# Kernel tuning notes

Hardware: AMD Instinct MI355X
Metric: run time of the kernel (lower is better)

## Reference

```python
import jax, jax.numpy as jnp
import numpy as np

B, T, D = 2, 512, 1024
H = 16
DH = D // H          # 64 head dim
E = 8                # experts
K = 2                # top-k routing
F = 4 * D            # expert hidden dim


def _layernorm(x, s, b, eps=1e-5):
    mu = jnp.mean(x, axis=-1, keepdims=True)
    var = jnp.var(x, axis=-1, keepdims=True)
    return (x - mu) * jax.lax.rsqrt(var + eps) * s + b


def setup_inputs() -> dict:
    key = jax.random.key(0)
    ks = jax.random.split(key, 16)
    sd = 0.02
    return {
        "x": jax.random.normal(ks[0], (B, T, D), jnp.float32),
        "text_state": jax.random.normal(ks[1], (B, D), jnp.float32),
        "ln1_s": jnp.ones((D,), jnp.float32),
        "ln1_b": jnp.zeros((D,), jnp.float32),
        "w_qkv": jax.random.normal(ks[2], (D, 3 * D), jnp.float32) * sd,
        "b_qkv": jnp.zeros((3 * D,), jnp.float32),
        "w_o": jax.random.normal(ks[3], (D, D), jnp.float32) * sd,
        "b_o": jnp.zeros((D,), jnp.float32),
        "rel_bias": jax.random.normal(ks[4], (H, 2 * T - 1), jnp.float32) * sd,
        "ln2_s": jnp.ones((D,), jnp.float32),
        "ln2_b": jnp.zeros((D,), jnp.float32),
        "w_txt": jax.random.normal(ks[5], (D, D), jnp.float32) * sd,
        "b_txt": jnp.zeros((D,), jnp.float32),
        "w_r": jax.random.normal(ks[6], (D, E), jnp.float32) * sd,
        "b_r": jnp.zeros((E,), jnp.float32),
        "w1": jax.random.normal(ks[7], (E, D, F), jnp.float32) * sd,
        "b1": jnp.zeros((E, F), jnp.float32),
        "w2": jax.random.normal(ks[8], (E, F, D), jnp.float32) * sd,
        "b2": jnp.zeros((E, D), jnp.float32),
    }


def reference(x, text_state, ln1_s, ln1_b, w_qkv, b_qkv, w_o, b_o, rel_bias,
              ln2_s, ln2_b, w_txt, b_txt, w_r, b_r, w1, b1, w2, b2):
    # ---- temporal-bias multi-head self-attention (pre-LN, residual) ----
    h = _layernorm(x, ln1_s, ln1_b)
    qkv = (h @ w_qkv + b_qkv).reshape(B, T, 3, H, DH)
    q, k, v = qkv[:, :, 0], qkv[:, :, 1], qkv[:, :, 2]       # [B,T,H,DH]
    scores = jnp.einsum("bthd,bshd->bhts", q, k) / np.sqrt(DH).astype(np.float32)
    idx = jnp.arange(T)
    rel = idx[None, :] - idx[:, None] + (T - 1)              # [T,T] in [0, 2T-2]
    scores = scores + rel_bias[:, rel][None]                 # broadcast [1,H,T,T]
    attn = jax.nn.softmax(scores, axis=-1)
    ctx = jnp.einsum("bhts,bshd->bthd", attn, v).reshape(B, T, D)
    x = x + ctx @ w_o + b_o

    # ---- top-k MoE feed-forward with text-conditioned router ----
    h2 = _layernorm(x, ln2_s, ln2_b)
    router_in = h2 + (text_state @ w_txt + b_txt)[:, None, :]
    probs = jax.nn.softmax(router_in @ w_r + b_r, axis=-1)   # [B,T,E]
    topv, topi = jax.lax.top_k(probs, K)                     # [B,T,K]
    gates = topv / jnp.sum(topv, axis=-1, keepdims=True)
    gates_full = jnp.einsum("btk,btke->bte", gates, jax.nn.one_hot(topi, E, dtype=x.dtype))
    # dense grouped-expert compute, sparsely combined (same math as dispatch)
    hid = jax.nn.gelu(jnp.einsum("btd,edf->btef", h2, w1) + b1)      # [B,T,E,F]
    eout = jnp.einsum("btef,efd->bted", hid, w2) + b2                # [B,T,E,D]
    y = jnp.einsum("bte,bted->btd", gates_full, eout)
    x = x + y

    diag = jnp.mean(probs, axis=(0, 1))                      # expert load [E]
    return x, diag
```

## Files before the change

kernel.cpp:

```cpp
#include <hip/hip_runtime.h>
#include <hip/hip_bf16.h>
#include <math.h>

#define BB 2
#define TT 512
#define DD 1024
#define HH 16
#define DHH 64
#define EE 8
#define FF 4096
#define NTOK 1024
#define CAP 3072
#define SPL 2

typedef __attribute__((ext_vector_type(4))) float f32x4;
typedef __attribute__((ext_vector_type(8))) short short8;

__device__ __forceinline__ short f2b(float f) {
    __hip_bfloat16 h = __float2bfloat16(f);
    return *reinterpret_cast<short*>(&h);
}
__device__ __forceinline__ float b2f(short s) {
    __hip_bfloat16 h = *reinterpret_cast<__hip_bfloat16*>(&s);
    return __bfloat162float(h);
}

__device__ __forceinline__ void gload16(const short* g, short* l) {
    __builtin_amdgcn_global_load_lds((const __attribute__((address_space(1))) unsigned int*)g,
                                     (__attribute__((address_space(3))) unsigned int*)l,
                                     16, 0, 0);
}

template <int BF>
__global__ __launch_bounds__(256) void ln_kernel(const float* __restrict__ x,
                                                 const float* __restrict__ s,
                                                 const float* __restrict__ b,
                                                 void* __restrict__ outp) {
    int row = blockIdx.x;
    int tid = threadIdx.x;
    const float* xr = x + (size_t)row * DD;
    float sm = 0.f, sq = 0.f;
    for (int i = tid; i < DD; i += 256) {
        float v = xr[i];
        sm += v; sq += v * v;
    }
    #pragma unroll
    for (int o = 32; o; o >>= 1) {
        sm += __shfl_down(sm, o);
        sq += __shfl_down(sq, o);
    }
    __shared__ float r1[4], r2[4];
    if ((tid & 63) == 0) { r1[tid >> 6] = sm; r2[tid >> 6] = sq; }
    __syncthreads();
    float tot  = r1[0] + r1[1] + r1[2] + r1[3];
    float totq = r2[0] + r2[1] + r2[2] + r2[3];
    float mu  = tot * (1.f / DD);
    float var = totq * (1.f / DD) - mu * mu;
    float inv = rsqrtf(var + 1e-5f);
    for (int i = tid; i < DD; i += 256) {
        float v = (xr[i] - mu) * inv * s[i] + b[i];
        if (BF) ((short*)outp)[(size_t)row * DD + i] = f2b(v);
        else    ((float*)outp)[(size_t)row * DD + i] = v;
    }
}

__global__ __launch_bounds__(256) void transpose_cast(const float* __restrict__ src,
                                                      short* __restrict__ dst,
                                                      int K, int N) {
    __shared__ float t[64][65];
    src += (size_t)blockIdx.z * K * N;
    dst += (size_t)blockIdx.z * K * N;
    int k0 = blockIdx.y * 64, n0 = blockIdx.x * 64;
    int rr = threadIdx.x >> 4;
    int cc = (threadIdx.x & 15) * 4;
    #pragma unroll
    for (int p = 0; p < 4; p++) {
        float4 v = *(const float4*)&src[(size_t)(k0 + rr + p * 16) * N + n0 + cc];
        t[rr + p * 16][cc]     = v.x;
        t[rr + p * 16][cc + 1] = v.y;
        t[rr + p * 16][cc + 2] = v.z;
        t[rr + p * 16][cc + 3] = v.w;
    }
    __syncthreads();
    #pragma unroll
    for (int p = 0; p < 4; p++) {
        int n = rr + p * 16;
        short4 o;
        o.x = f2b(t[cc][n]); o.y = f2b(t[cc + 1][n]);
        o.z = f2b(t[cc + 2][n]); o.w = f2b(t[cc + 3][n]);
        *(short4*)&dst[(size_t)(n0 + n) * K + k0 + cc] = o;
    }
}

__global__ __launch_bounds__(256) void v_transpose(const short* __restrict__ Vb,
                                                   short* __restrict__ VTb) {
    __shared__ short t[32][33];
    int bh = blockIdx.z;
    const short* src = Vb + (size_t)bh * TT * DHH;
    short* dst = VTb + (size_t)bh * DHH * TT;
    int t0 = blockIdx.x * 32, d0 = blockIdx.y * 32;
    int tx = threadIdx.x & 31, ty = threadIdx.x >> 5;
    #pragma unroll
    for (int p = 0; p < 4; p++)
        t[ty + p * 8][tx] = src[(size_t)(t0 + ty + p * 8) * DHH + d0 + tx];
    __syncthreads();
    #pragma unroll
    for (int p = 0; p < 4; p++)
        dst[(size_t)(d0 + ty + p * 8) * TT + t0 + tx] = t[tx][ty + p * 8];
}

__device__ __forceinline__ void gemm_loop128(const short* __restrict__ A,
                                             const short* __restrict__ B,
                                             int K, int lda, int ldb,
                                             short* As, short* Bs,
                                             f32x4 acc[4][4], int m0, int n0, int tid) {
    int wave = tid >> 6, lane = tid & 63;
    int wr = wave >> 1, wc = wave & 1;
    int lrow = lane & 15, lk = lane >> 4;
    int srow = lane >> 3;
    int sslot = (lane & 7) ^ srow;
    const short* Agb = A + (size_t)(m0 + srow) * lda + sslot * 8;
    const short* Bgb = B + (size_t)(n0 + srow) * ldb + sslot * 8;
    for (int k0 = 0; k0 < K; k0 += 64) {
        #pragma unroll
        for (int p = 0; p < 4; p++) {
            int rg = (wave * 4 + p) * 8;
            gload16(Agb + (size_t)rg * lda + k0, As + rg * 64);
            gload16(Bgb + (size_t)rg * ldb + k0, Bs + rg * 64);
        }
        __syncthreads();
        #pragma unroll
        for (int kk = 0; kk < 2; kk++) {
            int q = kk * 4 + lk;
            short8 a[4], b[4];
            #pragma unroll
            for (int i = 0; i < 4; i++) {
                int r = wr * 64 + i * 16 + lrow;
                uint4 v = ((const uint4*)As)[r * 8 + (q ^ (r & 7))];
                a[i] = *(short8*)&v;
            }
            #pragma unroll
            for (int j = 0; j < 4; j++) {
                int r = wc * 64 + j * 16 + lrow;
                uint4 v = ((const uint4*)Bs)[r * 8 + (q ^ (r & 7))];
                b[j] = *(short8*)&v;
            }
            #pragma unroll
            for (int i = 0; i < 4; i++)
                #pragma unroll
                for (int j = 0; j < 4; j++)
                    acc[i][j] = __builtin_amdgcn_mfma_f32_16x16x32_bf16(a[i], b[j], acc[i][j], 0, 0, 0);
        }
        __syncthreads();
    }
}

__device__ __forceinline__ void gemm_loop64(const short* __restrict__ A,
                                            const short* __restrict__ B,
                                            int K, int lda, int ldb,
                                            short* As, short* Bs,
                                            f32x4 acc[2][2], int m0, int n0, int tid) {
    int wave = tid >> 6, lane = tid & 63;
    int wr = wave >> 1, wc = wave & 1;
    int lrow = lane & 15, lk = lane >> 4;
    int sr = tid >> 3, ss = tid & 7;
    int sswz = (ss ^ (sr & 7)) * 8;
    const short* Ag0 = A + (size_t)(m0 + sr) * lda + sswz;
    const short* Ag1 = A + (size_t)(m0 + sr + 32) * lda + sswz;
    const short* Bg0 = B + (size_t)(n0 + sr) * ldb + sswz;
    const short* Bg1 = B + (size_t)(n0 + sr + 32) * ldb + sswz;
    short* lA0 = As + wave * 512;
    short* lA1 = As + 2048 + wave * 512;
    short* lB0 = Bs + wave * 512;
    short* lB1 = Bs + 2048 + wave * 512;
    int nt = K >> 6;
    gload16(Ag0, lA0); gload16(Ag1, lA1);
    gload16(Bg0, lB0); gload16(Bg1, lB1);
    __syncthreads();
    for (int t = 0; t < nt; ++t) {
        int h = (t & 1) * 4096;
        if (t + 1 < nt) {
            int k0 = (t + 1) << 6;
            int hn = 4096 - h;
            gload16(Ag0 + k0, lA0 + hn); gload16(Ag1 + k0, lA1 + hn);
            gload16(Bg0 + k0, lB0 + hn); gload16(Bg1 + k0, lB1 + hn);
        }
        const uint4* Asc = (const uint4*)(As + h);
        const uint4* Bsc = (const uint4*)(Bs + h);
        #pragma unroll
        for (int kk = 0; kk < 2; kk++) {
            int slot = kk * 4 + lk;
// ... 39 lines not shown
    short* lA1 = As + 2048 + wave * 512;
    short* lB0 = Bs + wave * 512;
    short* lB1 = Bs + 2048 + wave * 512;
    short* lB2 = Bs + 4096 + wave * 512;
    short* lB3 = Bs + 6144 + wave * 512;
    int nt = K >> 6;
    gload16(Ag0, lA0); gload16(Ag1, lA1);
    gload16(Bg0, lB0); gload16(Bg1, lB1);
    gload16(Bg2, lB2); gload16(Bg3, lB3);
    __syncthreads();
    for (int t = 0; t < nt; ++t) {
        int hA = (t & 1) * 4096;
        int hB = (t & 1) * 8192;
        if (t + 1 < nt) {
            int k0 = (t + 1) << 6;
            int hnA = 4096 - hA, hnB = 8192 - hB;
            gload16(Ag0 + k0, lA0 + hnA); gload16(Ag1 + k0, lA1 + hnA);
            gload16(Bg0 + k0, lB0 + hnB); gload16(Bg1 + k0, lB1 + hnB);
            gload16(Bg2 + k0, lB2 + hnB); gload16(Bg3 + k0, lB3 + hnB);
        }
        const uint4* Asc = (const uint4*)(As + hA);
        const uint4* Bsc = (const uint4*)(Bs + hB);
        #pragma unroll
        for (int kk = 0; kk < 2; kk++) {
            int slot = kk * 4 + lk;
            short8 a[2], b[4];
            #pragma unroll
            for (int i = 0; i < 2; i++) {
                int row = wr * 32 + i * 16 + lrow;
                uint4 v = Asc[row * 8 + (slot ^ (row & 7))];
                a[i] = *(short8*)&v;
            }
            #pragma unroll
            for (int j = 0; j < 4; j++) {
                int row = wc * 64 + j * 16 + lrow;
                uint4 v = Bsc[row * 8 + (slot ^ (row & 7))];
                b[j] = *(short8*)&v;
            }
            #pragma unroll
            for (int i = 0; i < 2; i++)
                #pragma unroll
                for (int j = 0; j < 4; j++)
                    acc[i][j] = __builtin_amdgcn_mfma_f32_16x16x32_bf16(a[i], b[j], acc[i][j], 0, 0, 0);
        }
        __syncthreads();
    }
}

__global__ __launch_bounds__(256) void gemm64_res_mfma(const short* __restrict__ A,
                                                       const short* __restrict__ Bw,
                                                       const float* __restrict__ bias,
                                                       const float* __restrict__ res,
                                                       float* __restrict__ C,
                                                       int N, int K) {
    __shared__ short As[8192];
    __shared__ short Bs[8192];
    int tid = threadIdx.x;
    int m0 = blockIdx.y * 64, n0 = blockIdx.x * 64;
    f32x4 acc[2][2] = {};
    gemm_loop64(A, Bw, K, K, K, As, Bs, acc, m0, n0, tid);
    int wave = tid >> 6, lane = tid & 63;
    int wr = wave >> 1, wc = wave & 1;
    int lrow = lane & 15, lk = lane >> 4;
    #pragma unroll
    for (int i = 0; i < 2; i++) {
        #pragma unroll
        for (int j = 0; j < 2; j++) {
            int col = n0 + wc * 32 + j * 16 + lrow;
            float bv = bias[col];
            #pragma unroll
            for (int r = 0; r < 4; r++) {
                int row = m0 + wr * 32 + i * 16 + lk * 4 + r;
                C[(size_t)row * N + col] = acc[i][j][r] + bv + res[(size_t)row * N + col];
            }
        }
    }
}

__global__ __launch_bounds__(256) void qkv_mfma(const short* __restrict__ A,
                                                const short* __restrict__ Bw,
                                                const float* __restrict__ bias,
                                                short* __restrict__ Qb,
                                                short* __restrict__ Kb,
                                                short* __restrict__ Vb) {
    __shared__ short As[8192];
    __shared__ short Bs[16384];
    int tid = threadIdx.x;
    int m0 = blockIdx.y * 64, n0 = blockIdx.x * 128;
    f32x4 acc[2][4] = {};
    gemm_loop_w(A, Bw, DD, As, Bs, acc, m0, n0, tid);
    int wave = tid >> 6, lane = tid & 63;
    int wr = wave >> 1, wc = wave & 1;
    int lrow = lane & 15, lk = lane >> 4;
    #pragma unroll
    for (int i = 0; i < 2; i++) {
        #pragma unroll
        for (int j = 0; j < 4; j++) {
            int col = n0 + wc * 64 + j * 16 + lrow;
            int part = col >> 10;
            int rem = col & 1023;
            int h = rem >> 6, d = rem & 63;
            short* dst = (part == 0) ? Qb : ((part == 1) ? Kb : Vb);
            float bv = bias[col];
            #pragma unroll
            for (int r = 0; r < 4; r++) {
                int row = m0 + wr * 32 + i * 16 + lk * 4 + r;
                int b = row >> 9, t = row & (TT - 1);
                dst[(((size_t)(b * HH + h)) * TT + t) * DHH + d] = f2b(acc[i][j][r] + bv);
            }
        }
    }
}

__global__ __launch_bounds__(256) void scores_mfma(const short* __restrict__ Qb,
                                                   const short* __restrict__ Kb,
                                                   float* __restrict__ S) {
    __shared__ short As[8192];
    __shared__ short Bs[16384];
    int tid = threadIdx.x;
    int bh = blockIdx.z;
    const short* A = Qb + (size_t)bh * TT * DHH;
    const short* B = Kb + (size_t)bh * TT * DHH;
    float* Sp = S + (size_t)bh * TT * TT;
    int m0 = blockIdx.y * 64, n0 = blockIdx.x * 128;
    f32x4 acc[2][4] = {};
    gemm_loop_w(A, B, DHH, As, Bs, acc, m0, n0, tid);
    int wave = tid >> 6, lane = tid & 63;
    int wr = wave >> 1, wc = wave & 1;
    int lrow = lane & 15, lk = lane >> 4;
    #pragma unroll
    for (int i = 0; i < 2; i++)
        #pragma unroll
        for (int j = 0; j < 4; j++) {
            int col = n0 + wc * 64 + j * 16 + lrow;
            #pragma unroll
            for (int r = 0; r < 4; r++) {
                int row = m0 + wr * 32 + i * 16 + lk * 4 + r;
                Sp[(size_t)row * TT + col] = acc[i][j][r];
            }
        }
}

__global__ __launch_bounds__(256) void softmax_kernel(const float* __restrict__ S,
                                                      const float* __restrict__ rel_bias,
                                                      short* __restrict__ P) {
    int row = blockIdx.x * 4 + (threadIdx.x >> 6);
    int lane = threadIdx.x & 63;
    int t = row & (TT - 1), h = (row >> 9) & (HH - 1);
    const float* Sr = S + (size_t)row * TT;
    const float* br = rel_bias + h * (2 * TT - 1) + (TT - 1) - t;
    float v[8];
    float mx = -1e30f;
    #pragma unroll
    for (int i = 0; i < 8; i++) {
        int s = lane + i * 64;
        v[i] = Sr[s] * 0.125f + br[s];
        mx = fmaxf(mx, v[i]);
    }
    #pragma unroll
    for (int o = 32; o; o >>= 1) mx = fmaxf(mx, __shfl_xor(mx, o));
    float sum = 0.f;
    #pragma unroll
    for (int i = 0; i < 8; i++) { v[i] = expf(v[i] - mx); sum += v[i]; }
    #pragma unroll
    for (int o = 32; o; o >>= 1) sum += __shfl_xor(sum, o);
    float inv = 1.f / sum;
    #pragma unroll
    for (int i = 0; i < 8; i++)
        P[(size_t)row * TT + lane + i * 64] = f2b(v[i] * inv);
}

__global__ __launch_bounds__(256) void pv_mfma(const short* __restrict__ P,
                                               const short* __restrict__ VTb,
                                               short* __restrict__ ctxb) {
    __shared__ short As[8192];
    __shared__ short Bs[8192];
    int tid = threadIdx.x;
    int bh = blockIdx.z;
    int h = bh & (HH - 1), b = bh >> 4;
    const short* A = P + (size_t)bh * TT * TT;
    const short* B = VTb + (size_t)bh * DHH * TT;
    int m0 = blockIdx.y * 64;
    f32x4 acc[2][2] = {};
    gemm_loop64(A, B, TT, TT, TT, As, Bs, acc, m0, 0, tid);
    int wave = tid >> 6, lane = tid & 63;
    int wr = wave >> 1, wc = wave & 1;
    int lrow = lane & 15, lk = lane >> 4;
    #pragma unroll
    for (int i = 0; i < 2; i++)
        #pragma unroll
        for (int j = 0; j < 2; j++) {
            int d = wc * 32 + j * 16 + lrow;
            #pragma unroll
            for (int r = 0; r < 4; r++) {
                int row = m0 + wr * 32 + i * 16 + lk * 4 + r;
                ctxb[((size_t)(b * TT + row)) * DD + h * DHH + d] = f2b(acc[i][j][r]);
            }
        }
}

__global__ __launch_bounds__(256) void moe_gemm1_mfma(const short* __restrict__ Ag,
                                                      const short* __restrict__ W1t,
                                                      const float* __restrict__ b1,
                                                      const int* __restrict__ counts,
                                                      const int* __restrict__ offs,
                                                      short* __restrict__ hid) {
    int e = blockIdx.y >> 4, tile = blockIdx.y & 15;
    int cnt = counts[e];
    int pcnt = (cnt + 127) & ~127;
    int row0 = tile * 128;
    if (row0 >= pcnt) return;
    int base = offs[e];
    const short* A  = Ag + (size_t)base * DD;
    const short* Bw = W1t + (size_t)e * FF * DD;
    __shared__ short As[8192];
    __shared__ short Bs[8192];
    int tid = threadIdx.x;
    int n0 = blockIdx.x * 128;
    f32x4 acc[4][4] = {};
    gemm_loop128(A, Bw, DD, DD, DD, As, Bs, acc, row0, n0, tid);
    int wave = tid >> 6, lane = tid & 63;
    int wr = wave >> 1, wc = wave & 1;
    int lrow = lane & 15, lk = lane >> 4;
    #pragma unroll
    for (int i = 0; i < 4; i++) {
        #pragma unroll
        for (int j = 0; j < 4; j++) {
            int col = n0 + wc * 64 + j * 16 + lrow;
            float bv = b1[e * FF + col];
            #pragma unroll
            for (int r = 0; r < 4; r++) {
                int row = row0 + wr * 64 + i * 16 + lk * 4 + r;
                float v = acc[i][j][r] + bv;
                float u = 0.7978845608028654f * (v + 0.044715f * v * v * v);
                float g = 0.5f * v * (1.f + tanhf(u));
                hid[(size_t)(base + row) * FF + col] = f2b(g);
            }
        }
    }
}

__global__ __launch_bounds__(256) void moe_gemm2_mfma(const short* __restrict__ hid,
                                                      const short* __restrict__ W2t,
                                                      const float* __restrict__ b2,
                                                      const float* __restrict__ pair_gate,
                                                      const int* __restrict__ counts,
                                                      const int* __restrict__ offs,
                                                      short* __restrict__ pair_part) {
    int s = blockIdx.z;
    int e = blockIdx.y >> 4, tile = blockIdx.y & 15;
    int cnt = counts[e];
    int pcnt = (cnt + 127) & ~127;
    int row0 = tile * 128;
    if (row0 >= pcnt) return;
    int base = offs[e];
    const int KS = FF / SPL;
    const short* A  = hid + (size_t)base * FF + s * KS;
    const short* Bw = W2t + (size_t)e * DD * FF + s * KS;
    __shared__ short As[8192];
    __shared__ short Bs[8192];
    int tid = threadIdx.x;
    int n0 = blockIdx.x * 128;
    f32x4 acc[4][4] = {};
    gemm_loop128(A, Bw, KS, FF, FF, As, Bs, acc, row0, n0, tid);
    int wave = tid >> 6, lane = tid & 63;
    int wr = wave >> 1, wc = wave & 1;
    int lrow = lane & 15, lk = lane >> 4;
    #pragma unroll
    for (int i = 0; i < 4; i++) {
        #pragma unroll
        for (int j = 0; j < 4; j++) {
            int col = n0 + wc * 64 + j * 16 + lrow;
            float bv = (s == 0) ? b2[e * DD + col] : 0.f;
            #pragma unroll
            for (int r = 0; r < 4; r++) {
                int row = row0 + wr * 64 + i * 16 + lk * 4 + r;
                float g = pair_gate[base + row];
                pair_part[((size_t)s * CAP + base + row) * DD + col] = f2b(g * (acc[i][j][r] + bv));
            }
        }
    }
}

__global__ __launch_bounds__(256) void txt_kernel(const float* __restrict__ ts,
                                                  const float* __restrict__ w,
                                                  const float* __restrict__ bias,
                                                  float* __restrict__ out) {
    int b = blockIdx.y;
    int col = blockIdx.x * 32 + (threadIdx.x & 31);
    int dg = threadIdx.x >> 5;
    float acc = 0.f;
    for (int d = dg * 128; d < dg * 128 + 128; d++)
        acc += ts[b * DD + d] * w[(size_t)d * DD + col];
    __shared__ float red[8][32];
    red[dg][threadIdx.x & 31] = acc;
    __syncthreads();
    if (threadIdx.x < 32) {
        float s = 0.f;
        #pragma unroll
        for (int g = 0; g < 8; g++) s += red[g][threadIdx.x];
        out[b * DD + col] = s + bias[col];
    }
}

__global__ __launch_bounds__(256) void router_kernel(const float* __restrict__ h2,
                                                     const float* __restrict__ txt,
                                                     const float* __restrict__ w_r,
                                                     const float* __restrict__ b_r,
                                                     float* __restrict__ probs,
                                                     float* __restrict__ gates,
                                                     int* __restrict__ counts) {
    int row = blockIdx.x;
    int b = row >> 9;
    int tid = threadIdx.x;
    float acc[EE] = {};
    for (int d = tid; d < DD; d += 256) {
        float r = h2[(size_t)row * DD + d] + txt[b * DD + d];
        #pragma unroll
        for (int e = 0; e < EE; e++) acc[e] += r * w_r[d * EE + e];
    }
    #pragma unroll
    for (int e = 0; e < EE; e++)
        #pragma unroll
        for (int o = 32; o; o >>= 1) acc[e] += __shfl_down(acc[e], o);
    __shared__ float lds[4][EE];
    int lane = tid & 63, w = tid >> 6;
    if (lane == 0)
        for (int e = 0; e < EE; e++) lds[w][e] = acc[e];
    __syncthreads();
    if (tid == 0) {
        float lg[EE], p[EE];
        float mx = -1e30f;
        for (int e = 0; e < EE; e++) {
            lg[e] = lds[0][e] + lds[1][e] + lds[2][e] + lds[3][e] + b_r[e];
            mx = fmaxf(mx, lg[e]);
        }
        float sum = 0.f;
        for (int e = 0; e < EE; e++) { p[e] = expf(lg[e] - mx); sum += p[e]; }
        float invs = 1.f / sum;
        for (int e = 0; e < EE; e++) { p[e] *= invs; probs[row * EE + e] = p[e]; }
        int i1 = 0;
        for (int e = 1; e < EE; e++) if (p[e] > p[i1]) i1 = e;
        int i2 = (i1 == 0) ? 1 : 0;
        for (int e = 0; e < EE; e++) if (e != i1 && p[e] > p[i2]) i2 = e;
        float gs = p[i1] + p[i2];
        for (int e = 0; e < EE; e++) gates[row * EE + e] = 0.f;
        gates[row * EE + i1] = p[i1] / gs;
        gates[row * EE + i2] = p[i2] / gs;
        atomicAdd(&counts[i1], 1);
        atomicAdd(&counts[i2], 1);
    }
}

__global__ void offs_kernel(const int* __restrict__ counts, int* __restrict__ offs) {
    if (threadIdx.x == 0) {
        int acc = 0;
        for (int e = 0; e < EE; e++) { offs[e] = acc; acc += (counts[e] + 127) & ~127; }
    }
}

__global__ __launch_bounds__(256) void scatter_kernel(const float* __restrict__ gates,
                                                      const int* __restrict__ offs,
                                                      int* __restrict__ fill,
                                                      int* __restrict__ tok_pos,
                                                      float* __restrict__ pair_gate) {
    int t = blockIdx.x * 256 + threadIdx.x;
    if (t >= NTOK) return;
    int slot = 0;
    for (int e = 0; e < EE; e++) {
        float g = gates[t * EE + e];
        if (g > 0.f) {
            int pos = offs[e] + atomicAdd(&fill[e], 1);
            tok_pos[t * 2 + slot] = pos;
            pair_gate[pos] = g;
            slot++;
        }
    }
}

__global__ __launch_bounds__(256) void gather_tokens(const float* __restrict__ h2,
                                                     const int* __restrict__ tok_pos,
                                                     short* __restrict__ Ag) {
    int i = blockIdx.x;
    int pos = tok_pos[i];
    int t = i >> 1;
    int d = threadIdx.x * 4;
    #pragma unroll
    for (int k = 0; k < 4; k++)
        Ag[(size_t)pos * DD + d + k] = f2b(h2[(size_t)t * DD + d + k]);
}

__global__ __launch_bounds__(256) void diag_kernel(const float* __restrict__ probs,
                                                   float* __restrict__ out) {
    int e = blockIdx.x;
    int tid = threadIdx.x;
    float s = 0.f;
    for (int t = tid; t < NTOK; t += 256) s += probs[t * EE + e];
    #pragma unroll
    for (int o = 32; o; o >>= 1) s += __shfl_down(s, o);
    __shared__ float red[4];
    if ((tid & 63) == 0) red[tid >> 6] = s;
    __syncthreads();
    if (tid == 0) out[e] = (red[0] + red[1] + red[2] + red[3]) * (1.f / NTOK);
}

__global__ __launch_bounds__(256) void finaladd_kernel(float* __restrict__ out,
                                                       const short* __restrict__ pair_part,
                                                       const int* __restrict__ tok_pos) {
    int t = blockIdx.x;
    int d = threadIdx.x * 4;
    float4 a = *(const float4*)&out[(size_t)t * DD + d];
    #pragma unroll
    for (int sl = 0; sl < 2; sl++) {
        int pos = tok_pos[2 * t + sl];
        #pragma unroll
        for (int s = 0; s < SPL; s++) {
            short4 v = *(const short4*)&pair_part[((size_t)s * CAP + pos) * DD + d];
            a.x += b2f(v.x); a.y += b2f(v.y); a.z += b2f(v.z); a.w += b2f(v.w);
        }
    }
    *(float4*)&out[(size_t)t * DD + d] = a;
}

extern "C" void kernel_launch(void* const* d_in, const int* in_sizes, int n_in,
                              void* d_out, int out_size, void* d_ws, size_t ws_size,
                              hipStream_t stream) {
    const float* x          = (const float*)d_in[0];
    const float* text_state = (const float*)d_in[1];
    const float* ln1_s      = (const float*)d_in[2];
    const float* ln1_b      = (const float*)d_in[3];
    const float* w_qkv      = (const float*)d_in[4];
    const float* b_qkv      = (const float*)d_in[5];
    const float* w_o        = (const float*)d_in[6];
    const float* b_o        = (const float*)d_in[7];
    const float* rel_bias   = (const float*)d_in[8];
    const float* ln2_s      = (const float*)d_in[9];
    const float* ln2_b      = (const float*)d_in[10];
    const float* w_txt      = (const float*)d_in[11];
    const float* b_txt      = (const float*)d_in[12];
    const float* w_r        = (const float*)d_in[13];
    const float* b_r        = (const float*)d_in[14];
    const float* w1         = (const float*)d_in[15];
    const float* b1         = (const float*)d_in[16];
    const float* w2         = (const float*)d_in[17];
    const float* b2         = (const float*)d_in[18];

    float* out = (float*)d_out;

    char* p = (char*)d_ws;
    auto alloc = [&](size_t bytes) { char* r = p; p += (bytes + 255) & ~(size_t)255; return r; };
    short* h1b      = (short*)alloc((size_t)NTOK * DD * 2);
    short* Qb       = (short*)alloc((size_t)NTOK * DD * 2);
    short* Kb       = (short*)alloc((size_t)NTOK * DD * 2);
    short* Vb       = (short*)alloc((size_t)NTOK * DD * 2);
    short* VTb      = (short*)alloc((size_t)NTOK * DD * 2);
    char*  region1  = alloc((size_t)BB * HH * TT * TT * 4);
    char*  region2  = alloc((size_t)BB * HH * TT * TT * 2);
    short* ctxb     = (short*)alloc((size_t)NTOK * DD * 2);
    float* h2       = (float*)alloc((size_t)NTOK * DD * 4);
    float* txt      = (float*)alloc((size_t)BB * DD * 4);
    float* probs    = (float*)alloc((size_t)NTOK * EE * 4);
    float* gates    = (float*)alloc((size_t)NTOK * EE * 4);
    float* pair_gate= (float*)alloc((size_t)CAP * 4);
    int*   counts   = (int*)alloc(8 * 4);
    int*   fill     = (int*)alloc(8 * 4);
    int*   offs     = (int*)alloc(8 * 4);
    int*   tok_pos  = (int*)alloc((size_t)NTOK * 2 * 4);
    short* wqkvT    = (short*)alloc((size_t)3 * DD * DD * 2);
    short* woT      = (short*)alloc((size_t)DD * DD * 2);
    short* w1T      = (short*)alloc((size_t)EE * FF * DD * 2);
    short* w2T      = (short*)alloc((size_t)EE * DD * FF * 2);

    float* S         = (float*)region1;
    short* P         = (short*)region2;
    short* Ag        = (short*)region1;
    short* hid       = (short*)(region1 + (((size_t)CAP * DD * 2 + 255) & ~(size_t)255));
    short* pair_part = (short*)region2;

    transpose_cast<<<dim3(3 * DD / 64, DD / 64, 1), 256, 0, stream>>>(w_qkv, wqkvT, DD, 3 * DD);
    transpose_cast<<<dim3(DD / 64, DD / 64, 1), 256, 0, stream>>>(w_o, woT, DD, DD);
    transpose_cast<<<dim3(FF / 64, DD / 64, EE), 256, 0, stream>>>(w1, w1T, DD, FF);
    transpose_cast<<<dim3(DD / 64, FF / 64, EE), 256, 0, stream>>>(w2, w2T, FF, DD);

    ln_kernel<1><<<NTOK, 256, 0, stream>>>(x, ln1_s, ln1_b, h1b);
    qkv_mfma<<<dim3(3 * DD / 128, NTOK / 64), 256, 0, stream>>>(h1b, wqkvT, b_qkv, Qb, Kb, Vb);
    v_transpose<<<dim3(TT / 32, DHH / 32, BB * HH), 256, 0, stream>>>(Vb, VTb);
    scores_mfma<<<dim3(TT / 128, TT / 64, BB * HH), 256, 0, stream>>>(Qb, Kb, S);
    softmax_kernel<<<BB * HH * TT / 4, 256, 0, stream>>>(S, rel_bias, P);
    pv_mfma<<<dim3(1, TT / 64, BB * HH), 256, 0, stream>>>(P, VTb, ctxb);
    gemm64_res_mfma<<<dim3(DD / 64, NTOK / 64), 256, 0, stream>>>(ctxb, woT, b_o, x, out, DD, DD);
    ln_kernel<0><<<NTOK, 256, 0, stream>>>(out, ln2_s, ln2_b, h2);
    txt_kernel<<<dim3(DD / 32, BB), 256, 0, stream>>>(text_state, w_txt, b_txt, txt);
    hipMemsetAsync(counts, 0, 8 * 4, stream);
    hipMemsetAsync(fill, 0, 8 * 4, stream);
    hipMemsetAsync(Ag, 0, (size_t)CAP * DD * 2, stream);
    router_kernel<<<NTOK, 256, 0, stream>>>(h2, txt, w_r, b_r, probs, gates, counts);
    offs_kernel<<<1, 64, 0, stream>>>(counts, offs);
    scatter_kernel<<<NTOK / 256, 256, 0, stream>>>(gates, offs, fill, tok_pos, pair_gate);
    gather_tokens<<<NTOK * 2, 256, 0, stream>>>(h2, tok_pos, Ag);
    diag_kernel<<<EE, 256, 0, stream>>>(probs, out + (size_t)NTOK * DD);
    moe_gemm1_mfma<<<dim3(FF / 128, EE * 16), 256, 0, stream>>>(Ag, w1T, b1, counts, offs, hid);
    moe_gemm2_mfma<<<dim3(DD / 128, EE * 16, SPL), 256, 0, stream>>>(hid, w2T, b2, pair_gate, counts, offs, pair_part);
    finaladd_kernel<<<NTOK, 256, 0, stream>>>(out, pair_part, tok_pos);
}
```

Before: 335.9 us.

## Fuse prep kernels, scores+softmax, V transpose into QKV epilogue, and MoE bookkeeping

```diff
diff --git a/kernel.cpp b/kernel.cpp
--- a/kernel.cpp
+++ b/kernel.cpp
@@ -31,82 +31,115 @@
                                      16, 0, 0);
 }
 
-template <int BF>
-__global__ __launch_bounds__(256) void ln_kernel(const float* __restrict__ x,
-                                                 const float* __restrict__ s,
-                                                 const float* __restrict__ b,
-                                                 void* __restrict__ outp) {
-    int row = blockIdx.x;
-    int tid = threadIdx.x;
-    const float* xr = x + (size_t)row * DD;
-    float sm = 0.f, sq = 0.f;
-    for (int i = tid; i < DD; i += 256) {
-        float v = xr[i];
-        sm += v; sq += v * v;
-    }
-    #pragma unroll
-    for (int o = 32; o; o >>= 1) {
-        sm += __shfl_down(sm, o);
-        sq += __shfl_down(sq, o);
-    }
-    __shared__ float r1[4], r2[4];
-    if ((tid & 63) == 0) { r1[tid >> 6] = sm; r2[tid >> 6] = sq; }
-    __syncthreads();
-    float tot  = r1[0] + r1[1] + r1[2] + r1[3];
-    float totq = r2[0] + r2[1] + r2[2] + r2[3];
-    float mu  = tot * (1.f / DD);
-    float var = totq * (1.f / DD) - mu * mu;
-    float inv = rsqrtf(var + 1e-5f);
-    for (int i = tid; i < DD; i += 256) {
-        float v = (xr[i] - mu) * inv * s[i] + b[i];
-        if (BF) ((short*)outp)[(size_t)row * DD + i] = f2b(v);
-        else    ((float*)outp)[(size_t)row * DD + i] = v;
-    }
-}
-
-__global__ __launch_bounds__(256) void transpose_cast(const float* __restrict__ src,
-                                                      short* __restrict__ dst,
-                                                      int K, int N) {
-    __shared__ float t[64][65];
-    src += (size_t)blockIdx.z * K * N;
-    dst += (size_t)blockIdx.z * K * N;
-    int k0 = blockIdx.y * 64, n0 = blockIdx.x * 64;
-    int rr = threadIdx.x >> 4;
-    int cc = (threadIdx.x & 15) * 4;
+__device__ __forceinline__ int seg_base(const int* counts, int e) {
+    int a = 0;
+    for (int i = 0; i < e; i++) a += (counts[i] + 127) & ~127;
+    return a;
+}
+
+__device__ __forceinline__ void tc_tile(const float* __restrict__ src, short* __restrict__ dst,
+                                        int K, int N, int k0, int n0, int tid, float* sm) {
+    int rr = tid >> 4;
+    int cc = (tid & 15) * 4;
     #pragma unroll
     for (int p = 0; p < 4; p++) {
         float4 v = *(const float4*)&src[(size_t)(k0 + rr + p * 16) * N + n0 + cc];
-        t[rr + p * 16][cc]     = v.x;
-        t[rr + p * 16][cc + 1] = v.y;
-        t[rr + p * 16][cc + 2] = v.z;
-        t[rr + p * 16][cc + 3] = v.w;
+        sm[(rr + p * 16) * 65 + cc]     = v.x;
+        sm[(rr + p * 16) * 65 + cc + 1] = v.y;
+        sm[(rr + p * 16) * 65 + cc + 2] = v.z;
+        sm[(rr + p * 16) * 65 + cc + 3] = v.w;
     }
     __syncthreads();
     #pragma unroll
     for (int p = 0; p < 4; p++) {
         int n = rr + p * 16;
         short4 o;
-        o.x = f2b(t[cc][n]); o.y = f2b(t[cc + 1][n]);
-        o.z = f2b(t[cc + 2][n]); o.w = f2b(t[cc + 3][n]);
+        o.x = f2b(sm[cc * 65 + n]);       o.y = f2b(sm[(cc + 1) * 65 + n]);
+        o.z = f2b(sm[(cc + 2) * 65 + n]); o.w = f2b(sm[(cc + 3) * 65 + n]);
         *(short4*)&dst[(size_t)(n0 + n) * K + k0 + cc] = o;
     }
 }
 
-__global__ __launch_bounds__(256) void v_transpose(const short* __restrict__ Vb,
-                                                   short* __restrict__ VTb) {
-    __shared__ short t[32][33];
-    int bh = blockIdx.z;
-    const short* src = Vb + (size_t)bh * TT * DHH;
-    short* dst = VTb + (size_t)bh * DHH * TT;
-    int t0 = blockIdx.x * 32, d0 = blockIdx.y * 32;
-    int tx = threadIdx.x & 31, ty = threadIdx.x >> 5;
-    #pragma unroll
-    for (int p = 0; p < 4; p++)
-        t[ty + p * 8][tx] = src[(size_t)(t0 + ty + p * 8) * DHH + d0 + tx];
+__device__ __forceinline__ void ln_row_bf16(const float* __restrict__ x, const float* __restrict__ s,
+                                            const float* __restrict__ bsc, short* __restrict__ out,
+                                            int row, int tid, float* sm) {
+    const float* xr = x + (size_t)row * DD;
+    float smv = 0.f, sq = 0.f;
+    for (int i = tid; i < DD; i += 256) { float v = xr[i]; smv += v; sq += v * v; }
+    #pragma unroll
+    for (int o = 32; o; o >>= 1) { smv += __shfl_down(smv, o); sq += __shfl_down(sq, o); }
+    if ((tid & 63) == 0) { sm[tid >> 6] = smv; sm[4 + (tid >> 6)] = sq; }
     __syncthreads();
-    #pragma unroll
-    for (int p = 0; p < 4; p++)
-        dst[(size_t)(d0 + ty + p * 8) * TT + t0 + tx] = t[tx][ty + p * 8];
+    float tot = sm[0] + sm[1] + sm[2] + sm[3];
+    float totq = sm[4] + sm[5] + sm[6] + sm[7];
+    float mu = tot * (1.f / DD);
+    float var = totq * (1.f / DD) - mu * mu;
+    float inv = rsqrtf(var + 1e-5f);
+    for (int i = tid; i < DD; i += 256)
+        out[(size_t)row * DD + i] = f2b((xr[i] - mu) * inv * s[i] + bsc[i]);
+}
+
+__device__ __forceinline__ void txt_blk(const float* __restrict__ ts, const float* __restrict__ w,
+                                        const float* __restrict__ bias, float* __restrict__ out,
+                                        int b, int colblk, int tid, float* sm) {
+    int col = colblk * 32 + (tid & 31);
+    int dg = tid >> 5;
+    float acc = 0.f;
+    for (int d = dg * 128; d < dg * 128 + 128; d++)
+        acc += ts[b * DD + d] * w[(size_t)d * DD + col];
+    sm[dg * 32 + (tid & 31)] = acc;
+    __syncthreads();
+    if (tid < 32) {
+        float s2 = 0.f;
+        #pragma unroll
+        for (int g = 0; g < 8; g++) s2 += sm[g * 32 + tid];
+        out[b * DD + col] = s2 + bias[col];
+    }
+}
+
+#define PREP_QKV   768
+#define PREP_WO    1024
+#define PREP_W1    9216
+#define PREP_W2    17408
+#define PREP_LN    18432
+#define PREP_TXT   18496
+
+__global__ __launch_bounds__(256) void prep_kernel(const float* __restrict__ w_qkv,
+                                                   const float* __restrict__ w_o,
+                                                   const float* __restrict__ w1,
+                                                   const float* __restrict__ w2,
+                                                   const float* __restrict__ x,
+                                                   const float* __restrict__ ln1_s,
+                                                   const float* __restrict__ ln1_b,
+                                                   const float* __restrict__ ts,
+                                                   const float* __restrict__ w_txt,
+                                                   const float* __restrict__ b_txt,
+                                                   short* __restrict__ wqkvT,
+                                                   short* __restrict__ woT,
+                                                   short* __restrict__ w1T,
+                                                   short* __restrict__ w2T,
+                                                   short* __restrict__ h1b,
+                                                   float* __restrict__ txt) {
+    __shared__ float sm[64 * 65];
+    int idx = blockIdx.x, tid = threadIdx.x;
+    if (idx < PREP_QKV) {
+        int bx = idx % 48, by = idx / 48;
+        tc_tile(w_qkv, wqkvT, DD, 3 * DD, by * 64, bx * 64, tid, sm);
+    } else if (idx < PREP_WO) {
+        int r = idx - PREP_QKV; int bx = r % 16, by = r / 16;
+        tc_tile(w_o, woT, DD, DD, by * 64, bx * 64, tid, sm);
+    } else if (idx < PREP_W1) {
+        int r = idx - PREP_WO; int e = r >> 10; r &= 1023; int bx = r % 64, by = r / 64;
+        tc_tile(w1 + (size_t)e * DD * FF, w1T + (size_t)e * FF * DD, DD, FF, by * 64, bx * 64, tid, sm);
+    } else if (idx < PREP_W2) {
+        int r = idx - PREP_W1; int e = r >> 10; r &= 1023; int bx = r % 16, by = r / 16;
+        tc_tile(w2 + (size_t)e * FF * DD, w2T + (size_t)e * DD * FF, FF, DD, by * 64, bx * 64, tid, sm);
+    } else if (idx < PREP_LN) {
+        ln_row_bf16(x, ln1_s, ln1_b, h1b, idx - PREP_W2, tid, sm);
+    } else {
+        int r = idx - PREP_LN; int b = r >> 5, colblk = r & 31;
+        txt_blk(ts, w_txt, b_txt, txt, b, colblk, tid, sm);
+    }
 }
 
 __device__ __forceinline__ void gemm_loop128(const short* __restrict__ A,
@@ -312,7 +345,7 @@
                                                 const float* __restrict__ bias,
                                                 short* __restrict__ Qb,
                                                 short* __restrict__ Kb,
-                                                short* __restrict__ Vb) {
+                                                short* __restrict__ VTb) {
     __shared__ short As[8192];
     __shared__ short Bs[16384];
     int tid = threadIdx.x;
@@ -330,74 +363,146 @@
             int part = col >> 10;
             int rem = col & 1023;
             int h = rem >> 6, d = rem & 63;
-            short* dst = (part == 0) ? Qb : ((part == 1) ? Kb : Vb);
             float bv = bias[col];
             #pragma unroll
             for (int r = 0; r < 4; r++) {
                 int row = m0 + wr * 32 + i * 16 + lk * 4 + r;
                 int b = row >> 9, t = row & (TT - 1);
-                dst[(((size_t)(b * HH + h)) * TT + t) * DHH + d] = f2b(acc[i][j][r] + bv);
-            }
-        }
-    }
-}
-
-__global__ __launch_bounds__(256) void scores_mfma(const short* __restrict__ Qb,
-                                                   const short* __restrict__ Kb,
-                                                   float* __restrict__ S) {
-    __shared__ short As[8192];
-    __shared__ short Bs[16384];
+                short val = f2b(acc[i][j][r] + bv);
+                if (part == 0)      Qb[(((size_t)(b * HH + h)) * TT + t) * DHH + d] = val;
+                else if (part == 1) Kb[(((size_t)(b * HH + h)) * TT + t) * DHH + d] = val;
+                else                VTb[((size_t)(b * HH + h) * DHH + d) * TT + t] = val;
+            }
+        }
+    }
+}
+
+__global__ __launch_bounds__(256) void scores_softmax(const short* __restrict__ Qb,
+                                                      const short* __restrict__ Kb,
+                                                      const float* __restrict__ rel_bias,
+                                                      short* __restrict__ P) {
+    __shared__ short As[64 * 64];
+    __shared__ short Bs[128 * 64];
+    __shared__ float red_m[64][2];
+    __shared__ float red_s[64][2];
     int tid = threadIdx.x;
-    int bh = blockIdx.z;
-    const short* A = Qb + (size_t)bh * TT * DHH;
-    const short* B = Kb + (size_t)bh * TT * DHH;
-    float* Sp = S + (size_t)bh * TT * TT;
-    int m0 = blockIdx.y * 64, n0 = blockIdx.x * 128;
-    f32x4 acc[2][4] = {};
-    gemm_loop_w(A, B, DHH, As, Bs, acc, m0, n0, tid);
+    int bh = blockIdx.y, h = bh & (HH - 1);
+    int m0 = blockIdx.x * 64;
+    const short* A  = Qb + (size_t)bh * TT * DHH;
+    const short* Bk = Kb + (size_t)bh * TT * DHH;
     int wave = tid >> 6, lane = tid & 63;
     int wr = wave >> 1, wc = wave & 1;
-    int lrow = lane & 15, lk = lane >> 4;
-    #pragma unroll
-    for (int i = 0; i < 2; i++)
-        #pragma unroll
-        for (int j = 0; j < 4; j++) {
-            int col = n0 + wc * 64 + j * 16 + lrow;
-            #pragma unroll
-            for (int r = 0; r < 4; r++) {
-                int row = m0 + wr * 32 + i * 16 + lk * 4 + r;
-                Sp[(size_t)row * TT + col] = acc[i][j][r];
-            }
-        }
-}
-
-__global__ __launch_bounds__(256) void softmax_kernel(const float* __restrict__ S,
-                                                      const float* __restrict__ rel_bias,
-                                                      short* __restrict__ P) {
-    int row = blockIdx.x * 4 + (threadIdx.x >> 6);
-    int lane = threadIdx.x & 63;
-    int t = row & (TT - 1), h = (row >> 9) & (HH - 1);
-    const float* Sr = S + (size_t)row * TT;
-    const float* br = rel_bias + h * (2 * TT - 1) + (TT - 1) - t;
-    float v[8];
-    float mx = -1e30f;
-    #pragma unroll
-    for (int i = 0; i < 8; i++) {
-        int s = lane + i * 64;
-        v[i] = Sr[s] * 0.125f + br[s];
-        mx = fmaxf(mx, v[i]);
-    }
-    #pragma unroll
-    for (int o = 32; o; o >>= 1) mx = fmaxf(mx, __shfl_xor(mx, o));
-    float sum = 0.f;
-    #pragma unroll
-    for (int i = 0; i < 8; i++) { v[i] = expf(v[i] - mx); sum += v[i]; }
-    #pragma unroll
-    for (int o = 32; o; o >>= 1) sum += __shfl_xor(sum, o);
-    float inv = 1.f / sum;
-    #pragma unroll
-    for (int i = 0; i < 8; i++)
-        P[(size_t)row * TT + lane + i * 64] = f2b(v[i] * inv);
+    int l15 = lane & 15, lk = lane >> 4;
+    int srow = lane >> 3;
+    int sslot = (lane & 7) ^ srow;
+    const short* Aq = A + (size_t)(m0 + srow) * DHH + sslot * 8;
+    #pragma unroll
+    for (int p2 = 0; p2 < 2; p2++) {
+        int rg = (wave * 2 + p2) * 8;
+        gload16(Aq + (size_t)rg * DHH, As + rg * 64);
+    }
+    f32x4 acc[4][2][4] = {};
+    const short* Bb = Bk + (size_t)srow * DHH + sslot * 8;
+    #pragma unroll
+    for (int c = 0; c < 4; c++) {
+        #pragma unroll
+        for (int p = 0; p < 4; p++) {
+            int rg = (wave * 4 + p) * 8;
+            gload16(Bb + (size_t)(c * 128 + rg) * DHH, Bs + rg * 64);
+        }
+        __syncthreads();
+        #pragma unroll
+        for (int kk = 0; kk < 2; kk++) {
+            int q = kk * 4 + lk;
+            short8 a[2], b[4];
+            #pragma unroll
+            for (int i = 0; i < 2; i++) {
+                int r = wr * 32 + i * 16 + l15;
+                uint4 v = ((const uint4*)As)[r * 8 + (q ^ (r & 7))];
+                a[i] = *(short8*)&v;
+            }
+            #pragma unroll
+            for (int j = 0; j < 4; j++) {
+                int r = wc * 64 + j * 16 + l15;
+                uint4 v = ((const uint4*)Bs)[r * 8 + (q ^ (r & 7))];
+                b[j] = *(short8*)&v;
+            }
+            #pragma unroll
+            for (int i = 0; i < 2; i++)
+                #pragma unroll
+                for (int j = 0; j < 4; j++)
+                    acc[c][i][j] = __builtin_amdgcn_mfma_f32_16x16x32_bf16(a[i], b[j], acc[c][i][j], 0, 0, 0);
+        }
+        __syncthreads();
+    }
+    int lk4 = lk * 4;
+    const float* rb = rel_bias + h * (2 * TT - 1);
+    #pragma unroll
+    for (int i = 0; i < 2; i++) {
+        #pragma unroll
+        for (int r = 0; r < 4; r++) {
+            int rowl = wr * 32 + i * 16 + lk4 + r;
+            int bbase = 511 - m0 - rowl;
+            float mx = -1e30f;
+            #pragma unroll
+            for (int c = 0; c < 4; c++) {
+                #pragma unroll
+                for (int j = 0; j < 4; j++) {
+                    int col = c * 128 + wc * 64 + j * 16 + l15;
+                    float v = acc[c][i][j][r] * 0.125f + rb[bbase + col];
+                    acc[c][i][j][r] = v;
+                    mx = fmaxf(mx, v);
+                }
+            }
+            mx = fmaxf(mx, __shfl_xor(mx, 1));
+            mx = fmaxf(mx, __shfl_xor(mx, 2));
+            mx = fmaxf(mx, __shfl_xor(mx, 4));
+            mx = fmaxf(mx, __shfl_xor(mx, 8));
+            if (l15 == 0) red_m[rowl][wc] = mx;
+        }
+    }
+    __syncthreads();
+    #pragma unroll
+    for (int i = 0; i < 2; i++) {
+        #pragma unroll
+        for (int r = 0; r < 4; r++) {
+            int rowl = wr * 32 + i * 16 + lk4 + r;
+            float m = fmaxf(red_m[rowl][0], red_m[rowl][1]);
+            float s = 0.f;
+            #pragma unroll
+            for (int c = 0; c < 4; c++) {
+                #pragma unroll
+                for (int j = 0; j < 4; j++) {
+                    float e = __expf(acc[c][i][j][r] - m);
+                    acc[c][i][j][r] = e;
+                    s += e;
+                }
+            }
+            s += __shfl_xor(s, 1);
+            s += __shfl_xor(s, 2);
+            s += __shfl_xor(s, 4);
+            s += __shfl_xor(s, 8);
+            if (l15 == 0) red_s[rowl][wc] = s;
+        }
+    }
+    __syncthreads();
+    short* Pp = P + (size_t)bh * TT * TT;
+    #pragma unroll
+    for (int i = 0; i < 2; i++) {
+        #pragma unroll
+        for (int r = 0; r < 4; r++) {
+            int rowl = wr * 32 + i * 16 + lk4 + r;
+            float inv = 1.f / (red_s[rowl][0] + red_s[rowl][1]);
+            #pragma unroll
+            for (int c = 0; c < 4; c++) {
+                #pragma unroll
+                for (int j = 0; j < 4; j++) {
+                    int col = c * 128 + wc * 64 + j * 16 + l15;
+                    Pp[(size_t)(m0 + rowl) * TT + col] = f2b(acc[c][i][j][r] * inv);
+                }
+            }
+        }
+    }
 }
 
 __global__ __launch_bounds__(256) void pv_mfma(const short* __restrict__ P,
@@ -429,108 +534,27 @@
         }
 }
 
-__global__ __launch_bounds__(256) void moe_gemm1_mfma(const short* __restrict__ Ag,
-                                                      const short* __restrict__ W1t,
-                                                      const float* __restrict__ b1,
-                                                      const int* __restrict__ counts,
-                                                      const int* __restrict__ offs,
-                                                      short* __restrict__ hid) {
-    int e = blockIdx.y >> 4, tile = blockIdx.y & 15;
-    int cnt = counts[e];
-    int pcnt = (cnt + 127) & ~127;
-    int row0 = tile * 128;
-    if (row0 >= pcnt) return;
-    int base = offs[e];
-    const short* A  = Ag + (size_t)base * DD;
-    const short* Bw = W1t + (size_t)e * FF * DD;
-    __shared__ short As[8192];
-    __shared__ short Bs[8192];
+__global__ __launch_bounds__(256) void ln_kernel_f32(const float* __restrict__ x,
+                                                     const float* __restrict__ s,
+                                                     const float* __restrict__ b,
+                                                     float* __restrict__ outp) {
+    int row = blockIdx.x;
     int tid = threadIdx.x;
-    int n0 = blockIdx.x * 128;
-    f32x4 acc[4][4] = {};
-    gemm_loop128(A, Bw, DD, DD, DD, As, Bs, acc, row0, n0, tid);
-    int wave = tid >> 6, lane = tid & 63;
-    int wr = wave >> 1, wc = wave & 1;
-    int lrow = lane & 15, lk = lane >> 4;
-    #pragma unroll
-    for (int i = 0; i < 4; i++) {
-        #pragma unroll
-        for (int j = 0; j < 4; j++) {
-            int col = n0 + wc * 64 + j * 16 + lrow;
-            float bv = b1[e * FF + col];
-            #pragma unroll
-            for (int r = 0; r < 4; r++) {
-                int row = row0 + wr * 64 + i * 16 + lk * 4 + r;
-                float v = acc[i][j][r] + bv;
-                float u = 0.7978845608028654f * (v + 0.044715f * v * v * v);
-                float g = 0.5f * v * (1.f + tanhf(u));
-                hid[(size_t)(base + row) * FF + col] = f2b(g);
-            }
-        }
-    }
-}
-
-__global__ __launch_bounds__(256) void moe_gemm2_mfma(const short* __restrict__ hid,
-                                                      const short* __restrict__ W2t,
-                                                      const float* __restrict__ b2,
-                                                      const float* __restrict__ pair_gate,
-                                                      const int* __restrict__ counts,
-                                                      const int* __restrict__ offs,
-                                                      short* __restrict__ pair_part) {
-    int s = blockIdx.z;
-    int e = blockIdx.y >> 4, tile = blockIdx.y & 15;
-    int cnt = counts[e];
-    int pcnt = (cnt + 127) & ~127;
-    int row0 = tile * 128;
-    if (row0 >= pcnt) return;
-    int base = offs[e];
-    const int KS = FF / SPL;
-    const short* A  = hid + (size_t)base * FF + s * KS;
-    const short* Bw = W2t + (size_t)e * DD * FF + s * KS;
-    __shared__ short As[8192];
-    __shared__ short Bs[8192];
-    int tid = threadIdx.x;
-    int n0 = blockIdx.x * 128;
-    f32x4 acc[4][4] = {};
-    gemm_loop128(A, Bw, KS, FF, FF, As, Bs, acc, row0, n0, tid);
-    int wave = tid >> 6, lane = tid & 63;
-    int wr = wave >> 1, wc = wave & 1;
-    int lrow = lane & 15, lk = lane >> 4;
-    #pragma unroll
-    for (int i = 0; i < 4; i++) {
-        #pragma unroll
-        for (int j = 0; j < 4; j++) {
-            int col = n0 + wc * 64 + j * 16 + lrow;
-            float bv = (s == 0) ? b2[e * DD + col] : 0.f;
-            #pragma unroll
-            for (int r = 0; r < 4; r++) {
-                int row = row0 + wr * 64 + i * 16 + lk * 4 + r;
-                float g = pair_gate[base + row];
-                pair_part[((size_t)s * CAP + base + row) * DD + col] = f2b(g * (acc[i][j][r] + bv));
-            }
-        }
-    }
-}
-
-__global__ __launch_bounds__(256) void txt_kernel(const float* __restrict__ ts,
-                                                  const float* __restrict__ w,
-                                                  const float* __restrict__ bias,
-                                                  float* __restrict__ out) {
-    int b = blockIdx.y;
-    int col = blockIdx.x * 32 + (threadIdx.x & 31);
-    int dg = threadIdx.x >> 5;
-    float acc = 0.f;
-    for (int d = dg * 128; d < dg * 128 + 128; d++)
-        acc += ts[b * DD + d] * w[(size_t)d * DD + col];
-    __shared__ float red[8][32];
-    red[dg][threadIdx.x & 31] = acc;
+    const float* xr = x + (size_t)row * DD;
+    float sm = 0.f, sq = 0.f;
+    for (int i = tid; i < DD; i += 256) { float v = xr[i]; sm += v; sq += v * v; }
+    #pragma unroll
+    for (int o = 32; o; o >>= 1) { sm += __shfl_down(sm, o); sq += __shfl_down(sq, o); }
+    __shared__ float r1[4], r2[4];
+    if ((tid & 63) == 0) { r1[tid >> 6] = sm; r2[tid >> 6] = sq; }
     __syncthreads();
-    if (threadIdx.x < 32) {
-        float s = 0.f;
-        #pragma unroll
-        for (int g = 0; g < 8; g++) s += red[g][threadIdx.x];
-        out[b * DD + col] = s + bias[col];
-    }
+    float tot = r1[0] + r1[1] + r1[2] + r1[3];
+    float totq = r2[0] + r2[1] + r2[2] + r2[3];
+    float mu = tot * (1.f / DD);
+    float var = totq * (1.f / DD) - mu * mu;
+    float inv = rsqrtf(var + 1e-5f);
+    for (int i = tid; i < DD; i += 256)
+        outp[(size_t)row * DD + i] = (xr[i] - mu) * inv * s[i] + b[i];
 }
 
 __global__ __launch_bounds__(256) void router_kernel(const float* __restrict__ h2,
@@ -582,29 +606,43 @@
     }
 }
 
-__global__ void offs_kernel(const int* __restrict__ counts, int* __restrict__ offs) {
-    if (threadIdx.x == 0) {
-        int acc = 0;
-        for (int e = 0; e < EE; e++) { offs[e] = acc; acc += (counts[e] + 127) & ~127; }
-    }
-}
-
-__global__ __launch_bounds__(256) void scatter_kernel(const float* __restrict__ gates,
-                                                      const int* __restrict__ offs,
-                                                      int* __restrict__ fill,
-                                                      int* __restrict__ tok_pos,
-                                                      float* __restrict__ pair_gate) {
-    int t = blockIdx.x * 256 + threadIdx.x;
-    if (t >= NTOK) return;
-    int slot = 0;
-    for (int e = 0; e < EE; e++) {
-        float g = gates[t * EE + e];
-        if (g > 0.f) {
-            int pos = offs[e] + atomicAdd(&fill[e], 1);
-            tok_pos[t * 2 + slot] = pos;
-            pair_gate[pos] = g;
-            slot++;
-        }
+__global__ __launch_bounds__(256) void scatter_diag_kernel(const float* __restrict__ gates,
+                                                           const float* __restrict__ probs,
+                                                           const int* __restrict__ counts,
+                                                           int* __restrict__ fill,
+                                                           int* __restrict__ tok_pos,
+                                                           float* __restrict__ pair_gate,
+                                                           float* __restrict__ diag) {
+    int blk = blockIdx.x;
+    if (blk < 4) {
+        int t = blk * 256 + threadIdx.x;
+        int offs[EE];
+        {
+            int a = 0;
+            #pragma unroll
+            for (int e = 0; e < EE; e++) { offs[e] = a; a += (counts[e] + 127) & ~127; }
+        }
+        int slot = 0;
+        for (int e = 0; e < EE; e++) {
+            float g = gates[t * EE + e];
+            if (g > 0.f) {
+                int pos = offs[e] + atomicAdd(&fill[e], 1);
+                tok_pos[t * 2 + slot] = pos;
+                pair_gate[pos] = g;
+                slot++;
+            }
+        }
+    } else {
+        int e = blk - 4;
+        int tid = threadIdx.x;
+        float s = 0.f;
+        for (int t = tid; t < NTOK; t += 256) s += probs[t * EE + e];
+        #pragma unroll
+        for (int o = 32; o; o >>= 1) s += __shfl_down(s, o);
+        __shared__ float red[4];
+        if ((tid & 63) == 0) red[tid >> 6] = s;
+        __syncthreads();
+        if (tid == 0) diag[e] = (red[0] + red[1] + red[2] + red[3]) * (1.f / NTOK);
     }
 }
 
@@ -620,18 +658,85 @@
         Ag[(size_t)pos * DD + d + k] = f2b(h2[(size_t)t * DD + d + k]);
 }
 
-__global__ __launch_bounds__(256) void diag_kernel(const float* __restrict__ probs,
-                                                   float* __restrict__ out) {
-    int e = blockIdx.x;
+__global__ __launch_bounds__(256) void moe_gemm1_mfma(const short* __restrict__ Ag,
+                                                      const short* __restrict__ W1t,
+                                                      const float* __restrict__ b1,
+                                                      const int* __restrict__ counts,
+                                                      short* __restrict__ hid) {
+    int e = blockIdx.y >> 4, tile = blockIdx.y & 15;
+    int cnt = counts[e];
+    int pcnt = (cnt + 127) & ~127;
+    int row0 = tile * 128;
+    if (row0 >= pcnt) return;
+    int base = seg_base(counts, e);
+    const short* A  = Ag + (size_t)base * DD;
+    const short* Bw = W1t + (size_t)e * FF * DD;
+    __shared__ short As[8192];
+    __shared__ short Bs[8192];
     int tid = threadIdx.x;
-    float s = 0.f;
-    for (int t = tid; t < NTOK; t += 256) s += probs[t * EE + e];
-    #pragma unroll
-    for (int o = 32; o; o >>= 1) s += __shfl_down(s, o);
-    __shared__ float red[4];
-    if ((tid & 63) == 0) red[tid >> 6] = s;
-    __syncthreads();
-    if (tid == 0) out[e] = (red[0] + red[1] + red[2] + red[3]) * (1.f / NTOK);
+    int n0 = blockIdx.x * 128;
+    f32x4 acc[4][4] = {};
+    gemm_loop128(A, Bw, DD, DD, DD, As, Bs, acc, row0, n0, tid);
+    int wave = tid >> 6, lane = tid & 63;
+    int wr = wave >> 1, wc = wave & 1;
+    int lrow = lane & 15, lk = lane >> 4;
+    #pragma unroll
+    for (int i = 0; i < 4; i++) {
+        #pragma unroll
+        for (int j = 0; j < 4; j++) {
+            int col = n0 + wc * 64 + j * 16 + lrow;
+            float bv = b1[e * FF + col];
+            #pragma unroll
+            for (int r = 0; r < 4; r++) {
+                int row = row0 + wr * 64 + i * 16 + lk * 4 + r;
+                float v = acc[i][j][r] + bv;
+                float u = 0.7978845608028654f * (v + 0.044715f * v * v * v);
+                float g = 0.5f * v * (1.f + tanhf(u));
+                hid[(size_t)(base + row) * FF + col] = f2b(g);
+            }
+        }
+    }
+}
+
+__global__ __launch_bounds__(256) void moe_gemm2_mfma(const short* __restrict__ hid,
+                                                      const short* __restrict__ W2t,
+                                                      const float* __restrict__ b2,
+                                                      const float* __restrict__ pair_gate,
+                                                      const int* __restrict__ counts,
+                                                      short* __restrict__ pair_part) {
+    int s = blockIdx.z;
+    int e = blockIdx.y >> 4, tile = blockIdx.y & 15;
+    int cnt = counts[e];
+    int pcnt = (cnt + 127) & ~127;
+    int row0 = tile * 128;
+    if (row0 >= pcnt) return;
+    int base = seg_base(counts, e);
+    const int KS = FF / SPL;
+    const short* A  = hid + (size_t)base * FF + s * KS;
+    const short* Bw = W2t + (size_t)e * DD * FF + s * KS;
+    __shared__ short As[8192];
+    __shared__ short Bs[8192];
+    int tid = threadIdx.x;
+    int n0 = blockIdx.x * 128;
+    f32x4 acc[4][4] = {};
+    gemm_loop128(A, Bw, KS, FF, FF, As, Bs, acc, row0, n0, tid);
+    int wave = tid >> 6, lane = tid & 63;
+    int wr = wave >> 1, wc = wave & 1;
+    int lrow = lane & 15, lk = lane >> 4;
+    #pragma unroll
+    for (int i = 0; i < 4; i++) {
+        #pragma unroll
+        for (int j = 0; j < 4; j++) {
+            int col = n0 + wc * 64 + j * 16 + lrow;
+            float bv = (s == 0) ? b2[e * DD + col] : 0.f;
+            #pragma unroll
+            for (int r = 0; r < 4; r++) {
+                int row = row0 + wr * 64 + i * 16 + lk * 4 + r;
+                float g = pair_gate[base + row];
+                pair_part[((size_t)s * CAP + base + row) * DD + col] = f2b(g * (acc[i][j][r] + bv));
+            }
+        }
+    }
 }
 
 __global__ __launch_bounds__(256) void finaladd_kernel(float* __restrict__ out,
@@ -682,9 +787,9 @@
     short* h1b      = (short*)alloc((size_t)NTOK * DD * 2);
     short* Qb       = (short*)alloc((size_t)NTOK * DD * 2);
     short* Kb       = (short*)alloc((size_t)NTOK * DD * 2);
-    short* Vb       = (short*)alloc((size_t)NTOK * DD * 2);
     short* VTb      = (short*)alloc((size_t)NTOK * DD * 2);
-    char*  region1  = alloc((size_t)BB * HH * TT * TT * 4);
+    short* Ag       = (short*)alloc((size_t)CAP * DD * 2);
+    short* hid      = (short*)alloc((size_t)CAP * FF * 2);
     char*  region2  = alloc((size_t)BB * HH * TT * TT * 2);
     short* ctxb     = (short*)alloc((size_t)NTOK * DD * 2);
     float* h2       = (float*)alloc((size_t)NTOK * DD * 4);
@@ -692,44 +797,32 @@
     float* probs    = (float*)alloc((size_t)NTOK * EE * 4);
     float* gates    = (float*)alloc((size_t)NTOK * EE * 4);
     float* pair_gate= (float*)alloc((size_t)CAP * 4);
-    int*   counts   = (int*)alloc(8 * 4);
-    int*   fill     = (int*)alloc(8 * 4);
-    int*   offs     = (int*)alloc(8 * 4);
+    int*   iflags   = (int*)alloc(512);
+    int*   counts   = iflags;
+    int*   fill     = iflags + 64;
     int*   tok_pos  = (int*)alloc((size_t)NTOK * 2 * 4);
     short* wqkvT    = (short*)alloc((size_t)3 * DD * DD * 2);
     short* woT      = (short*)alloc((size_t)DD * DD * 2);
     short* w1T      = (short*)alloc((size_t)EE * FF * DD * 2);
     short* w2T      = (short*)alloc((size_t)EE * DD * FF * 2);
 
-    float* S         = (float*)region1;
     short* P         = (short*)region2;
-    short* Ag        = (short*)region1;
-    short* hid       = (short*)(region1 + (((size_t)CAP * DD * 2 + 255) & ~(size_t)255));
     short* pair_part = (short*)region2;
 
-    transpose_cast<<<dim3(3 * DD / 64, DD / 64, 1), 256, 0, stream>>>(w_qkv, wqkvT, DD, 3 * DD);
-    transpose_cast<<<dim3(DD / 64, DD / 64, 1), 256, 0, stream>>>(w_o, woT, DD, DD);
-    transpose_cast<<<dim3(FF / 64, DD / 64, EE), 256, 0, stream>>>(w1, w1T, DD, FF);
-    transpose_cast<<<dim3(DD / 64, FF / 64, EE), 256, 0, stream>>>(w2, w2T, FF, DD);
-
-    ln_kernel<1><<<NTOK, 256, 0, stream>>>(x, ln1_s, ln1_b, h1b);
-    qkv_mfma<<<dim3(3 * DD / 128, NTOK / 64), 256, 0, stream>>>(h1b, wqkvT, b_qkv, Qb, Kb, Vb);
-    v_transpose<<<dim3(TT / 32, DHH / 32, BB * HH), 256, 0, stream>>>(Vb, VTb);
-    scores_mfma<<<dim3(TT / 128, TT / 64, BB * HH), 256, 0, stream>>>(Qb, Kb, S);
-    softmax_kernel<<<BB * HH * TT / 4, 256, 0, stream>>>(S, rel_bias, P);
+    prep_kernel<<<PREP_TXT, 256, 0, stream>>>(w_qkv, w_o, w1, w2, x, ln1_s, ln1_b,
+                                              text_state, w_txt, b_txt,
+                                              wqkvT, woT, w1T, w2T, h1b, txt);
+    hipMemsetAsync(iflags, 0, 512, stream);
+    qkv_mfma<<<dim3(3 * DD / 128, NTOK / 64), 256, 0, stream>>>(h1b, wqkvT, b_qkv, Qb, Kb, VTb);
+    scores_softmax<<<dim3(TT / 64, BB * HH), 256, 0, stream>>>(Qb, Kb, rel_bias, P);
     pv_mfma<<<dim3(1, TT / 64, BB * HH), 256, 0, stream>>>(P, VTb, ctxb);
     gemm64_res_mfma<<<dim3(DD / 64, NTOK / 64), 256, 0, stream>>>(ctxb, woT, b_o, x, out, DD, DD);
-    ln_kernel<0><<<NTOK, 256, 0, stream>>>(out, ln2_s, ln2_b, h2);
-    txt_kernel<<<dim3(DD / 32, BB), 256, 0, stream>>>(text_state, w_txt, b_txt, txt);
-    hipMemsetAsync(counts, 0, 8 * 4, stream);
-    hipMemsetAsync(fill, 0, 8 * 4, stream);
-    hipMemsetAsync(Ag, 0, (size_t)CAP * DD * 2, stream);
+    ln_kernel_f32<<<NTOK, 256, 0, stream>>>(out, ln2_s, ln2_b, h2);
     router_kernel<<<NTOK, 256, 0, stream>>>(h2, txt, w_r, b_r, probs, gates, counts);
-    offs_kernel<<<1, 64, 0, stream>>>(counts, offs);
-    scatter_kernel<<<NTOK / 256, 256, 0, stream>>>(gates, offs, fill, tok_pos, pair_gate);
+    scatter_diag_kernel<<<12, 256, 0, stream>>>(gates, probs, counts, fill, tok_pos,
+                                                pair_gate, out + (size_t)NTOK * DD);
     gather_tokens<<<NTOK * 2, 256, 0, stream>>>(h2, tok_pos, Ag);
-    diag_kernel<<<EE, 256, 0, stream>>>(probs, out + (size_t)NTOK * DD);
-    moe_gemm1_mfma<<<dim3(FF / 128, EE * 16), 256, 0, stream>>>(Ag, w1T, b1, counts, offs, hid);
-    moe_gemm2_mfma<<<dim3(DD / 128, EE * 16, SPL), 256, 0, stream>>>(hid, w2T, b2, pair_gate, counts, offs, pair_part);
+    moe_gemm1_mfma<<<dim3(FF / 128, EE * 16), 256, 0, stream>>>(Ag, w1T, b1, counts, hid);
+    moe_gemm2_mfma<<<dim3(DD / 128, EE * 16, SPL), 256, 0, stream>>>(hid, w2T, b2, pair_gate, counts, pair_part);
     finaladd_kernel<<<NTOK, 256, 0, stream>>>(out, pair_part, tok_pos);
 }
```

Result: slower. 349.6 us (+4.1%).
